# Kernel optimization log

Hardware: AMD Instinct MI355X
Metric: run time of the kernel (lower is better)

## Reference

```python
import jax, jax.numpy as jnp
import numpy as np

B, TK, NK, H = 64, 512, 256, 512

def _masked_renorm_softmax(scores, mask):
    # softmax over last dim, multiply by mask, renormalize (as in the torch code)
    p = jax.nn.softmax(scores, axis=-1) * mask
    return p / jnp.sum(p, axis=-1, keepdims=True)

def setup_inputs() -> dict:
    key = jax.random.key(0)
    ks = jax.random.split(key, 14)
    s = 0.02
    return {
        "s_t_hat": jax.random.normal(ks[0], (B, 2 * H), jnp.float32),
        "encoder_outputs_token": jax.random.normal(ks[1], (B, TK, H), jnp.float32),
        "encoder_outputs_node": jax.random.normal(ks[2], (B, NK, H), jnp.float32),
        "node_to_token": jax.random.randint(ks[3], (B, TK), 0, NK),
        "enc_padding_mask_token": jnp.ones((B, TK), jnp.float32),
        "enc_padding_mask_node": jnp.ones((B, NK), jnp.float32),
        "graph": jax.random.uniform(ks[4], (B, NK, NK), jnp.float32),
        "flow": jax.random.uniform(ks[5], (B, NK), jnp.float32),
        # parameters (Linear weights stored as [in, out]; x @ W == torch Linear)
        "W_c": jax.random.normal(ks[6], (H,), jnp.float32) * s,          # Linear(1, H)
        "W_tok": jax.random.normal(ks[7], (H, H), jnp.float32) * s,      # encode_proj_token
        "W_node": jax.random.normal(ks[8], (H, H), jnp.float32) * s,     # encode_proj_node
        "W_dec": jax.random.normal(ks[9], (2 * H, H), jnp.float32) * s,  # decode_proj
        "b_dec": jnp.zeros((H,), jnp.float32),
        "v_tok": jax.random.normal(ks[10], (H,), jnp.float32) * s,       # v_token
        "v_node": jax.random.normal(ks[11], (H,), jnp.float32) * s,      # v_node
    }

def reference(s_t_hat, encoder_outputs_token, encoder_outputs_node, node_to_token,
              enc_padding_mask_token, enc_padding_mask_node, graph, flow,
              W_c, W_tok, W_node, W_dec, b_dec, v_tok, v_node):
    # projections
    enc_tok_feat = jnp.einsum('bth,hk->btk', encoder_outputs_token, W_tok)   # [B,TK,H]
    enc_node_feat = jnp.einsum('bnh,hk->bnk', encoder_outputs_node, W_node)  # [B,NK,H]
    dec_fea = s_t_hat @ W_dec + b_dec                                        # [B,H]
    flow_feat = flow[..., None] * W_c                                        # [B,NK,H]

    # node attention
    e_node = jnp.tanh(enc_node_feat + dec_fea[:, None, :] + flow_feat)
    scores_node = jnp.einsum('bnh,h->bn', e_node, v_node)                    # [B,NK]
    attn_dist_node = _masked_renorm_softmax(scores_node, enc_padding_mask_node)

    # gather node attention onto tokens via node_to_token indices
    gathered = jnp.take_along_axis(attn_dist_node, node_to_token, axis=1)    # [B,TK]
    attn_dist_node_to_token = _masked_renorm_softmax(gathered, enc_padding_mask_token)

    # token attention
    e_tok = jnp.tanh(enc_tok_feat + dec_fea[:, None, :])
    scores_tok = jnp.einsum('bth,h->bt', e_tok, v_tok)                       # [B,TK]
    attn_dist_token = _masked_renorm_softmax(scores_tok, enc_padding_mask_token)

    # mix and context
    final_attn = 0.5 * attn_dist_token + 0.5 * attn_dist_node_to_token      # [B,TK]
    c_t = jnp.einsum('bt,bth->bh', final_attn, encoder_outputs_token)        # [B,H]

    # multi-hop graph diffusion of node attention
    zero_hop = attn_dist_node                                                # [B,NK]
    one_hop = jnp.einsum('bn,bnm->bm', zero_hop, graph)
    two_hop = jnp.einsum('bn,bnm->bm', one_hop, graph)
    flow_out = (zero_hop + one_hop + two_hop) * 0.33333

    return (c_t, final_attn, attn_dist_node, flow_out)
```

## Files before the change

### kernel.cpp

```cpp
#include <hip/hip_runtime.h>
#include <math.h>

constexpr int kB = 64;
constexpr int kTK = 512;
constexpr int kNK = 256;
constexpr int kH = 512;

typedef float f32x4 __attribute__((ext_vector_type(4)));
typedef __bf16 bf16x8 __attribute__((ext_vector_type(8)));

__device__ __forceinline__ unsigned short f32_to_bf16(float f) {
  unsigned int u = __float_as_uint(f);
  u += 0x7fffu + ((u >> 16) & 1u);
  return (unsigned short)(u >> 16);
}

__device__ __forceinline__ float tanh_fast(float x) {
  float e = __builtin_amdgcn_exp2f(x * 2.8853900817779268f);
  return 1.0f - 2.0f * __builtin_amdgcn_rcpf(e + 1.0f);
}

__global__ __launch_bounds__(256) void transpose_w_kernel(
    const float* __restrict__ Wtok, const float* __restrict__ Wnode,
    unsigned short* __restrict__ WtokT, unsigned short* __restrict__ WnodeT) {
  const float* W = blockIdx.z ? Wnode : Wtok;
  unsigned short* T = blockIdx.z ? WnodeT : WtokT;
  __shared__ float tile[32][33];
  const int tx = threadIdx.x, ty = threadIdx.y;
  const int bx = blockIdx.x, by = blockIdx.y;
#pragma unroll
  for (int i = 0; i < 4; ++i)
    tile[ty + 8 * i][tx] = W[(size_t)(by * 32 + ty + 8 * i) * kH + bx * 32 + tx];
  __syncthreads();
#pragma unroll
  for (int i = 0; i < 4; ++i)
    T[(size_t)(bx * 32 + ty + 8 * i) * kH + by * 32 + tx] =
        f32_to_bf16(tile[tx][ty + 8 * i]);
}

__global__ __launch_bounds__(512) void dec_fea_kernel(
    const float* __restrict__ s_t_hat, const float* __restrict__ W_dec,
    const float* __restrict__ b_dec, float* __restrict__ dec_fea) {
  __shared__ float sh[2 * kH];
  const int b = blockIdx.x, h = threadIdx.x;
  sh[h] = s_t_hat[(size_t)b * (2 * kH) + h];
  sh[h + kH] = s_t_hat[(size_t)b * (2 * kH) + kH + h];
  __syncthreads();
  float acc = 0.f;
#pragma unroll 16
  for (int k = 0; k < 2 * kH; ++k)
    acc = fmaf(sh[k], W_dec[(size_t)k * kH + h], acc);
  dec_fea[b * kH + h] = acc + b_dec[h];
}

template <int ROWS, bool IS_NODE>
__global__ __launch_bounds__(1024, 4) void scores_kernel(
    const float* __restrict__ A,
    const unsigned short* __restrict__ WT,
    const float* __restrict__ dec_fea,
    const float* __restrict__ flow,
    const float* __restrict__ W_c,
    const float* __restrict__ v,
    float* __restrict__ scores)
{
  constexpr int TILES_PER_B = ROWS / 64;
  const int b = blockIdx.x / TILES_PER_B;
  const int row0 = (blockIdx.x % TILES_PER_B) * 64;
  const int tid = threadIdx.x;
  const int wave = tid >> 6;
  const int lane = tid & 63;
  const int quad = lane >> 4;
  const int l15 = lane & 15;
  const int n0 = wave * 32;

  constexpr int LDA = 72;
  __shared__ __align__(16) unsigned short As[2 * 64 * LDA];
  __shared__ float red[16][64];

  const f32x4 fzero = {0.f, 0.f, 0.f, 0.f};
  f32x4 acc[4][2];
#pragma unroll
  for (int i = 0; i < 4; ++i)
#pragma unroll
    for (int j = 0; j < 2; ++j) acc[i][j] = fzero;

  const int r = tid >> 4;
  const int k0 = (tid & 15) * 4;
  const float* aptr = A + ((size_t)(b * ROWS + row0 + r)) * kH + k0;

  {
    float4 af = *(const float4*)(aptr);
    ushort4 ah;
    ah.x = f32_to_bf16(af.x); ah.y = f32_to_bf16(af.y);
    ah.z = f32_to_bf16(af.z); ah.w = f32_to_bf16(af.w);
    *(ushort4*)&As[r * LDA + k0] = ah;
  }

  const unsigned short* wt_base = WT + (size_t)(n0 + l15) * kH + quad * 8;

#pragma unroll 1
  for (int kc8 = 0; kc8 < 8; ++kc8) {
    __syncthreads();
    const unsigned short* Ac = As + (kc8 & 1) * (64 * LDA);

    bf16x8 bfr[2][2];
#pragma unroll
    for (int kh = 0; kh < 2; ++kh)
#pragma unroll
      for (int ni = 0; ni < 2; ++ni)
        bfr[kh][ni] = *(const bf16x8*)(wt_base + (size_t)(16 * ni) * kH +
                                       kc8 * 64 + kh * 32);

    bf16x8 afr[2][4];
#pragma unroll
    for (int kh = 0; kh < 2; ++kh)
#pragma unroll
      for (int mi = 0; mi < 4; ++mi)
        afr[kh][mi] =
            *(const bf16x8*)&Ac[(16 * mi + l15) * LDA + kh * 32 + quad * 8];

    if (kc8 < 7) {
      float4 af = *(const float4*)(aptr + (kc8 + 1) * 64);
      ushort4 ah;
      ah.x = f32_to_bf16(af.x); ah.y = f32_to_bf16(af.y);
      ah.z = f32_to_bf16(af.z); ah.w = f32_to_bf16(af.w);
      *(ushort4*)&As[((kc8 + 1) & 1) * (64 * LDA) + r * LDA + k0] = ah;
    }

#pragma unroll
    for (int kh = 0; kh < 2; ++kh)
#pragma unroll
      for (int mi = 0; mi < 4; ++mi)
#pragma unroll
        for (int ni = 0; ni < 2; ++ni)
          acc[mi][ni] = __builtin_amdgcn_mfma_f32_16x16x32_bf16(
              afr[kh][mi], bfr[kh][ni], acc[mi][ni], 0, 0, 0);
  }

  float dec2[2], vv2[2], wc2[2];
#pragma unroll
  for (int ni = 0; ni < 2; ++ni) {
    const int col = n0 + 16 * ni + l15;
    dec2[ni] = dec_fea[b * kH + col];
    vv2[ni] = v[col];
    if constexpr (IS_NODE) wc2[ni] = W_c[col]; else wc2[ni] = 0.f;
  }
#pragma unroll
  for (int mi = 0; mi < 4; ++mi) {
#pragma unroll
    for (int reg = 0; reg < 4; ++reg) {
      const int row = 16 * mi + quad * 4 + reg;
      float fl = 0.f;
      if constexpr (IS_NODE) fl = flow[b * kNK + row0 + row];
      float p = 0.f;
#pragma unroll
      for (int ni = 0; ni < 2; ++ni) {
        float val = acc[mi][ni][reg] + dec2[ni];
        if constexpr (IS_NODE) val = fmaf(fl, wc2[ni], val);
        p += tanh_fast(val) * vv2[ni];
      }
#pragma unroll
      for (int off = 1; off < 16; off <<= 1) p += __shfl_xor(p, off, 64);
      if (l15 == 0) red[wave][row] = p;
    }
  }
  __syncthreads();
  if (tid < 64) {
    float s = 0.f;
#pragma unroll
    for (int w = 0; w < 16; ++w) s += red[w][tid];
    scores[b * ROWS + row0 + tid] = s;
  }
}

__device__ __forceinline__ float block_max_512(float v, float* rbuf) {
#pragma unroll
  for (int off = 32; off >= 1; off >>= 1) v = fmaxf(v, __shfl_xor(v, off, 64));
  if ((threadIdx.x & 63) == 0) rbuf[threadIdx.x >> 6] = v;
  __syncthreads();
  float m = rbuf[0];
#pragma unroll
  for (int w = 1; w < 8; ++w) m = fmaxf(m, rbuf[w]);
  __syncthreads();
  return m;
}

__device__ __forceinline__ float block_sum_512(float v, float* rbuf) {
#pragma unroll
  for (int off = 32; off >= 1; off >>= 1) v += __shfl_xor(v, off, 64);
  if ((threadIdx.x & 63) == 0) rbuf[threadIdx.x >> 6] = v;
  __syncthreads();
  float s = rbuf[0];
#pragma unroll
  for (int w = 1; w < 8; ++w) s += rbuf[w];
  __syncthreads();
  return s;
}

__global__ __launch_bounds__(512) void softmax_mix_kernel(
    const float* __restrict__ scores_node, const float* __restrict__ scores_tok,
    const int* __restrict__ node_to_token,
    const float* __restrict__ mask_tok, const float* __restrict__ mask_node,
    float* __restrict__ out_final, float* __restrict__ out_attn_node) {
  const int b = blockIdx.x, tid = threadIdx.x;
  __shared__ float an_sh[kNK];
  __shared__ float rbuf[8];

  float sn = (tid < kNK) ? scores_node[b * kNK + tid] : -INFINITY;
  float m = block_max_512(sn, rbuf);
  float e = (tid < kNK) ? expf(sn - m) : 0.f;
  float s = block_sum_512(e, rbuf);
  float pm = (tid < kNK) ? (e / s) * mask_node[b * kNK + tid] : 0.f;
  float s2 = block_sum_512(pm, rbuf);
  float an = pm / s2;
  if (tid < kNK) {
    an_sh[tid] = an;
    out_attn_node[b * kNK + tid] = an;
  }
  __syncthreads();

  const float mt = mask_tok[b * kTK + tid];
  const int idx = node_to_token[b * kTK + tid];
  float g = an_sh[idx];
  float m2 = block_max_512(g, rbuf);
  float e2 = expf(g - m2);
  float sg = block_sum_512(e2, rbuf);
  float pg = (e2 / sg) * mt;
  float sg2 = block_sum_512(pg, rbuf);
  float an2t = pg / sg2;

  float st = scores_tok[b * kTK + tid];
  float m3 = block_max_512(st, rbuf);
  float e3 = expf(st - m3);
  float s3 = block_sum_512(e3, rbuf);
  float pt = (e3 / s3) * mt;
  float s32 = block_sum_512(pt, rbuf);
  float at = pt / s32;

  out_final[b * kTK + tid] = 0.5f * (at + an2t);
}

__global__ __launch_bounds__(512) void ct_partial_kernel(
    const float* __restrict__ final_attn, const float* __restrict__ enc_tok,
    float* __restrict__ ctp) {
  const int s = blockIdx.x, b = blockIdx.y, h = threadIdx.x;
  __shared__ float fa[128];
  if (h < 128) fa[h] = final_attn[b * kTK + s * 128 + h];
  __syncthreads();
  float acc = 0.f;
  const float* base = enc_tok + ((size_t)(b * kTK + s * 128)) * kH + h;
#pragma unroll 8
  for (int t = 0; t < 128; ++t)
    acc = fmaf(fa[t], base[(size_t)t * kH], acc);
  ctp[(size_t)(b * 4 + s) * kH + h] = acc;
}

__global__ __launch_bounds__(512) void ct_reduce_kernel(
    const float* __restrict__ ctp, float* __restrict__ out_ct) {
  const int b = blockIdx.x, h = threadIdx.x;
  float acc = 0.f;
#pragma unroll
  for (int s = 0; s < 4; ++s) acc += ctp[(size_t)(b * 4 + s) * kH + h];
  out_ct[b * kH + h] = acc;
}

__global__ __launch_bounds__(256) void flow1_kernel(
    const float* __restrict__ attn_node, const float* __restrict__ graph,
    float* __restrict__ fp1) {
  const int s = blockIdx.x, b = blockIdx.y, m = threadIdx.x;
  __shared__ float z[32];
  if (m < 32) z[m] = attn_node[b * kNK + s * 32 + m];
  __syncthreads();
  float acc = 0.f;
  const float* g = graph + ((size_t)(b * kNK + s * 32)) * kNK + m;
#pragma unroll 8
  for (int n = 0; n < 32; ++n) acc = fmaf(z[n], g[(size_t)n * kNK], acc);
  fp1[(b * 8 + s) * kNK + m] = acc;
}

__global__ __launch_bounds__(256) void flow3_kernel(
    const float* __restrict__ fp1, const float* __restrict__ graph,
    float* __restrict__ fp2) {
  const int s = blockIdx.x, b = blockIdx.y, m = threadIdx.x;
  __shared__ float one[32];
  if (m < 32) {
    float o = 0.f;
#pragma unroll
    for (int sp = 0; sp < 8; ++sp) o += fp1[(b * 8 + sp) * kNK + s * 32 + m];
    one[m] = o;
  }
  __syncthreads();
  float acc = 0.f;
  const float* g = graph + ((size_t)(b * kNK + s * 32)) * kNK + m;
#pragma unroll 8
  for (int n = 0; n < 32; ++n) acc = fmaf(one[n], g[(size_t)n * kNK], acc);
  fp2[(b * 8 + s) * kNK + m] = acc;
}

__global__ __launch_bounds__(256) void flow4_kernel(
    const float* __restrict__ fp1, const float* __restrict__ fp2,
    const float* __restrict__ attn_node, float* __restrict__ out_flow) {
  const int b = blockIdx.x, m = threadIdx.x;
  float one = 0.f, two = 0.f;
#pragma unroll
  for (int s = 0; s < 8; ++s) {
    one += fp1[(b * 8 + s) * kNK + m];
    two += fp2[(b * 8 + s) * kNK + m];
  }
  out_flow[b * kNK + m] = (attn_node[b * kNK + m] + one + two) * 0.33333f;
}

extern "C" void kernel_launch(void* const* d_in, const int* in_sizes, int n_in,
                              void* d_out, int out_size, void* d_ws, size_t ws_size,
                              hipStream_t stream) {
  (void)in_sizes; (void)n_in; (void)out_size; (void)ws_size;
  const float* s_t_hat  = (const float*)d_in[0];
  const float* enc_tok  = (const float*)d_in[1];
  const float* enc_node = (const float*)d_in[2];
  const int*   n2t      = (const int*)d_in[3];
  const float* mask_tok = (const float*)d_in[4];
  const float* mask_nd  = (const float*)d_in[5];
  const float* graph    = (const float*)d_in[6];
  const float* flow     = (const float*)d_in[7];
  const float* W_c      = (const float*)d_in[8];
  const float* W_tok    = (const float*)d_in[9];
  const float* W_node   = (const float*)d_in[10];
  const float* W_dec    = (const float*)d_in[11];
  const float* b_dec    = (const float*)d_in[12];
  const float* v_tok    = (const float*)d_in[13];
  const float* v_node   = (const float*)d_in[14];

  float* out = (float*)d_out;
  float* out_ct        = out;
  float* out_final     = out + kB * kH;
  float* out_attn_node = out + 2 * kB * kH;
  float* out_flow      = out_attn_node + kB * kNK;

  float* ws = (float*)d_ws;
  float* dec_fea_buf = ws;
  float* scores_tok  = ws + 32768;
  float* scores_node = ws + 65536;
  float* fp1         = ws + 81920;
  float* fp2         = ws + 81920 + 131072;
  unsigned short* WtokT  = (unsigned short*)(ws + 344064);
  unsigned short* WnodeT = WtokT + kH * kH;
  float* ctp = (float*)WtokT;

  transpose_w_kernel<<<dim3(16, 16, 2), dim3(32, 8), 0, stream>>>(
      W_tok, W_node, WtokT, WnodeT);
  dec_fea_kernel<<<kB, 512, 0, stream>>>(s_t_hat, W_dec, b_dec, dec_fea_buf);
  scores_kernel<kTK, false><<<kB * kTK / 64, 1024, 0, stream>>>(
      enc_tok, WtokT, dec_fea_buf, nullptr, nullptr, v_tok, scores_tok);
  scores_kernel<kNK, true><<<kB * kNK / 64, 1024, 0, stream>>>(
      enc_node, WnodeT, dec_fea_buf, flow, W_c, v_node, scores_node);
  softmax_mix_kernel<<<kB, 512, 0, stream>>>(scores_node, scores_tok, n2t,
                                             mask_tok, mask_nd, out_final, out_attn_node);
  ct_partial_kernel<<<dim3(4, kB), 512, 0, stream>>>(out_final, enc_tok, ctp);
  ct_reduce_kernel<<<kB, 512, 0, stream>>>(ctp, out_ct);
  flow1_kernel<<<dim3(8, kB), 256, 0, stream>>>(out_attn_node, graph, fp1);
  flow3_kernel<<<dim3(8, kB), 256, 0, stream>>>(fp1, graph, fp2);
  flow4_kernel<<<kB, 256, 0, stream>>>(fp1, fp2, out_attn_node, out_flow);
}
```

Before: 273.0 us.

## Retile score GEMM, split dec_fea matvec, drop softmax max passes, widen ct split

The scores kernel moves to 512 threads with each wave computing 64 output columns. It uses a fragment-ordered shared-memory layout for A and register double-buffers the B fragments, to raise per-wave reuse and overlap loads with MFMA work. The dec_fea matvec is split across 8 K-slices plus a reduce kernel for more parallelism. The c_t partial split goes from 4 to 8 slices. The softmax kernel drops the max-subtraction and the separate normalize-then-mask passes, folding the mask into one sum, which removes many block reductions but risks exp overflow for large scores.

```diff
diff --git a/kernel.cpp b/kernel.cpp
--- a/kernel.cpp
+++ b/kernel.cpp
@@ -8,6 +8,7 @@
 
 typedef float f32x4 __attribute__((ext_vector_type(4)));
 typedef __bf16 bf16x8 __attribute__((ext_vector_type(8)));
+typedef unsigned short u16x8 __attribute__((ext_vector_type(8)));
 
 __device__ __forceinline__ unsigned short f32_to_bf16(float f) {
   unsigned int u = __float_as_uint(f);
@@ -38,23 +39,32 @@
         f32_to_bf16(tile[tx][ty + 8 * i]);
 }
 
-__global__ __launch_bounds__(512) void dec_fea_kernel(
+__global__ __launch_bounds__(512) void dec_partial_kernel(
     const float* __restrict__ s_t_hat, const float* __restrict__ W_dec,
-    const float* __restrict__ b_dec, float* __restrict__ dec_fea) {
-  __shared__ float sh[2 * kH];
+    float* __restrict__ part) {
+  const int b = blockIdx.x, s = blockIdx.y, h = threadIdx.x;
+  __shared__ float sh[128];
+  if (h < 128) sh[h] = s_t_hat[(size_t)b * (2 * kH) + s * 128 + h];
+  __syncthreads();
+  float acc = 0.f;
+  const float* w = W_dec + (size_t)(s * 128) * kH + h;
+#pragma unroll 8
+  for (int k = 0; k < 128; ++k) acc = fmaf(sh[k], w[(size_t)k * kH], acc);
+  part[(size_t)(b * 8 + s) * kH + h] = acc;
+}
+
+__global__ __launch_bounds__(512) void dec_reduce_kernel(
+    const float* __restrict__ part, const float* __restrict__ b_dec,
+    float* __restrict__ dec_fea) {
   const int b = blockIdx.x, h = threadIdx.x;
-  sh[h] = s_t_hat[(size_t)b * (2 * kH) + h];
-  sh[h + kH] = s_t_hat[(size_t)b * (2 * kH) + kH + h];
-  __syncthreads();
-  float acc = 0.f;
-#pragma unroll 16
-  for (int k = 0; k < 2 * kH; ++k)
-    acc = fmaf(sh[k], W_dec[(size_t)k * kH + h], acc);
-  dec_fea[b * kH + h] = acc + b_dec[h];
+  float acc = b_dec[h];
+#pragma unroll
+  for (int s = 0; s < 8; ++s) acc += part[(size_t)(b * 8 + s) * kH + h];
+  dec_fea[b * kH + h] = acc;
 }
 
 template <int ROWS, bool IS_NODE>
-__global__ __launch_bounds__(1024, 4) void scores_kernel(
+__global__ __launch_bounds__(512, 2) void scores_kernel(
     const float* __restrict__ A,
     const unsigned short* __restrict__ WT,
     const float* __restrict__ dec_fea,
@@ -71,79 +81,86 @@
   const int lane = tid & 63;
   const int quad = lane >> 4;
   const int l15 = lane & 15;
-  const int n0 = wave * 32;
-
-  constexpr int LDA = 72;
-  __shared__ __align__(16) unsigned short As[2 * 64 * LDA];
-  __shared__ float red[16][64];
+  const int n0 = wave * 64;
+
+  __shared__ __align__(16) unsigned short As[2][4096];
+  __shared__ float red[8][64];
 
   const f32x4 fzero = {0.f, 0.f, 0.f, 0.f};
-  f32x4 acc[4][2];
+  f32x4 acc[4][4];
 #pragma unroll
   for (int i = 0; i < 4; ++i)
 #pragma unroll
-    for (int j = 0; j < 2; ++j) acc[i][j] = fzero;
-
-  const int r = tid >> 4;
-  const int k0 = (tid & 15) * 4;
-  const float* aptr = A + ((size_t)(b * ROWS + row0 + r)) * kH + k0;
-
-  {
-    float4 af = *(const float4*)(aptr);
-    ushort4 ah;
-    ah.x = f32_to_bf16(af.x); ah.y = f32_to_bf16(af.y);
-    ah.z = f32_to_bf16(af.z); ah.w = f32_to_bf16(af.w);
-    *(ushort4*)&As[r * LDA + k0] = ah;
-  }
-
-  const unsigned short* wt_base = WT + (size_t)(n0 + l15) * kH + quad * 8;
-
-#pragma unroll 1
-  for (int kc8 = 0; kc8 < 8; ++kc8) {
-    __syncthreads();
-    const unsigned short* Ac = As + (kc8 & 1) * (64 * LDA);
-
-    bf16x8 bfr[2][2];
+    for (int j = 0; j < 4; ++j) acc[i][j] = fzero;
+
+  const int sr = tid >> 3;
+  const int kq = tid & 7;
+  const int slot = (((kq >> 2) * 4 + (sr >> 4)) * 64 + (kq & 3) * 16 + (sr & 15)) * 8;
+  const float* aptr = A + ((size_t)(b * ROWS + row0 + sr)) * kH + kq * 8;
+
+  auto stage = [&](int kc, int buf) {
+    float4 a0 = *(const float4*)(aptr + kc * 64);
+    float4 a1 = *(const float4*)(aptr + kc * 64 + 4);
+    u16x8 h;
+    h[0] = f32_to_bf16(a0.x); h[1] = f32_to_bf16(a0.y);
+    h[2] = f32_to_bf16(a0.z); h[3] = f32_to_bf16(a0.w);
+    h[4] = f32_to_bf16(a1.x); h[5] = f32_to_bf16(a1.y);
+    h[6] = f32_to_bf16(a1.z); h[7] = f32_to_bf16(a1.w);
+    *(u16x8*)&As[buf][slot] = h;
+  };
+
+  const unsigned short* bbase = WT + (size_t)(n0 + l15) * kH + quad * 8;
+  auto load_b = [&](bf16x8 (&dst)[2][4], int kc) {
 #pragma unroll
     for (int kh = 0; kh < 2; ++kh)
 #pragma unroll
-      for (int ni = 0; ni < 2; ++ni)
-        bfr[kh][ni] = *(const bf16x8*)(wt_base + (size_t)(16 * ni) * kH +
-                                       kc8 * 64 + kh * 32);
-
+      for (int ni = 0; ni < 4; ++ni)
+        dst[kh][ni] =
+            *(const bf16x8*)(bbase + (size_t)(ni * 16) * kH + kc * 64 + kh * 32);
+  };
+
+  bf16x8 bcur[2][4];
+  stage(0, 0);
+  load_b(bcur, 0);
+  __syncthreads();
+
+#pragma unroll
+  for (int kc = 0; kc < 8; ++kc) {
+    bf16x8 bnxt[2][4];
+    if (kc < 7) {
+      load_b(bnxt, kc + 1);
+      stage(kc + 1, (kc + 1) & 1);
+    }
     bf16x8 afr[2][4];
 #pragma unroll
     for (int kh = 0; kh < 2; ++kh)
 #pragma unroll
       for (int mi = 0; mi < 4; ++mi)
-        afr[kh][mi] =
-            *(const bf16x8*)&Ac[(16 * mi + l15) * LDA + kh * 32 + quad * 8];
-
-    if (kc8 < 7) {
-      float4 af = *(const float4*)(aptr + (kc8 + 1) * 64);
-      ushort4 ah;
-      ah.x = f32_to_bf16(af.x); ah.y = f32_to_bf16(af.y);
-      ah.z = f32_to_bf16(af.z); ah.w = f32_to_bf16(af.w);
-      *(ushort4*)&As[((kc8 + 1) & 1) * (64 * LDA) + r * LDA + k0] = ah;
+        afr[kh][mi] = *(const bf16x8*)&As[kc & 1][((kh * 4 + mi) * 64 + lane) * 8];
+#pragma unroll
+    for (int kh = 0; kh < 2; ++kh)
+#pragma unroll
+      for (int mi = 0; mi < 4; ++mi)
+#pragma unroll
+        for (int ni = 0; ni < 4; ++ni)
+          acc[mi][ni] = __builtin_amdgcn_mfma_f32_16x16x32_bf16(
+              afr[kh][mi], bcur[kh][ni], acc[mi][ni], 0, 0, 0);
+    if (kc < 7) {
+#pragma unroll
+      for (int kh = 0; kh < 2; ++kh)
+#pragma unroll
+        for (int ni = 0; ni < 4; ++ni) bcur[kh][ni] = bnxt[kh][ni];
+      __syncthreads();
     }
-
-#pragma unroll
-    for (int kh = 0; kh < 2; ++kh)
-#pragma unroll
-      for (int mi = 0; mi < 4; ++mi)
-#pragma unroll
-        for (int ni = 0; ni < 2; ++ni)
-          acc[mi][ni] = __builtin_amdgcn_mfma_f32_16x16x32_bf16(
-              afr[kh][mi], bfr[kh][ni], acc[mi][ni], 0, 0, 0);
-  }
-
-  float dec2[2], vv2[2], wc2[2];
-#pragma unroll
-  for (int ni = 0; ni < 2; ++ni) {
+  }
+
+  float dec4[4], vv4[4], wc4[4];
+#pragma unroll
+  for (int ni = 0; ni < 4; ++ni) {
     const int col = n0 + 16 * ni + l15;
-    dec2[ni] = dec_fea[b * kH + col];
-    vv2[ni] = v[col];
-    if constexpr (IS_NODE) wc2[ni] = W_c[col]; else wc2[ni] = 0.f;
+    dec4[ni] = dec_fea[b * kH + col];
+    vv4[ni] = v[col];
+    if constexpr (IS_NODE) wc4[ni] = W_c[col]; else wc4[ni] = 0.f;
   }
 #pragma unroll
   for (int mi = 0; mi < 4; ++mi) {
@@ -154,10 +171,10 @@
       if constexpr (IS_NODE) fl = flow[b * kNK + row0 + row];
       float p = 0.f;
 #pragma unroll
-      for (int ni = 0; ni < 2; ++ni) {
-        float val = acc[mi][ni][reg] + dec2[ni];
-        if constexpr (IS_NODE) val = fmaf(fl, wc2[ni], val);
-        p += tanh_fast(val) * vv2[ni];
+      for (int ni = 0; ni < 4; ++ni) {
+        float val = acc[mi][ni][reg] + dec4[ni];
+        if constexpr (IS_NODE) val = fmaf(fl, wc4[ni], val);
+        p += tanh_fast(val) * vv4[ni];
       }
 #pragma unroll
       for (int off = 1; off < 16; off <<= 1) p += __shfl_xor(p, off, 64);
@@ -168,21 +185,9 @@
   if (tid < 64) {
     float s = 0.f;
 #pragma unroll
-    for (int w = 0; w < 16; ++w) s += red[w][tid];
+    for (int w = 0; w < 8; ++w) s += red[w][tid];
     scores[b * ROWS + row0 + tid] = s;
   }
-}
-
-__device__ __forceinline__ float block_max_512(float v, float* rbuf) {
-#pragma unroll
-  for (int off = 32; off >= 1; off >>= 1) v = fmaxf(v, __shfl_xor(v, off, 64));
-  if ((threadIdx.x & 63) == 0) rbuf[threadIdx.x >> 6] = v;
-  __syncthreads();
-  float m = rbuf[0];
-#pragma unroll
-  for (int w = 1; w < 8; ++w) m = fmaxf(m, rbuf[w]);
-  __syncthreads();
-  return m;
 }
 
 __device__ __forceinline__ float block_sum_512(float v, float* rbuf) {
@@ -206,13 +211,11 @@
   __shared__ float an_sh[kNK];
   __shared__ float rbuf[8];
 
-  float sn = (tid < kNK) ? scores_node[b * kNK + tid] : -INFINITY;
-  float m = block_max_512(sn, rbuf);
-  float e = (tid < kNK) ? expf(sn - m) : 0.f;
-  float s = block_sum_512(e, rbuf);
-  float pm = (tid < kNK) ? (e / s) * mask_node[b * kNK + tid] : 0.f;
-  float s2 = block_sum_512(pm, rbuf);
-  float an = pm / s2;
+  float en = 0.f;
+  if (tid < kNK)
+    en = expf(scores_node[b * kNK + tid]) * mask_node[b * kNK + tid];
+  float sn = block_sum_512(en, rbuf);
+  float an = en / sn;
   if (tid < kNK) {
     an_sh[tid] = an;
     out_attn_node[b * kNK + tid] = an;
@@ -221,21 +224,13 @@
 
   const float mt = mask_tok[b * kTK + tid];
   const int idx = node_to_token[b * kTK + tid];
-  float g = an_sh[idx];
-  float m2 = block_max_512(g, rbuf);
-  float e2 = expf(g - m2);
-  float sg = block_sum_512(e2, rbuf);
-  float pg = (e2 / sg) * mt;
-  float sg2 = block_sum_512(pg, rbuf);
-  float an2t = pg / sg2;
-
-  float st = scores_tok[b * kTK + tid];
-  float m3 = block_max_512(st, rbuf);
-  float e3 = expf(st - m3);
-  float s3 = block_sum_512(e3, rbuf);
-  float pt = (e3 / s3) * mt;
-  float s32 = block_sum_512(pt, rbuf);
-  float at = pt / s32;
+  float eg = expf(an_sh[idx]) * mt;
+  float sg = block_sum_512(eg, rbuf);
+  float an2t = eg / sg;
+
+  float et = expf(scores_tok[b * kTK + tid]) * mt;
+  float st = block_sum_512(et, rbuf);
+  float at = et / st;
 
   out_final[b * kTK + tid] = 0.5f * (at + an2t);
 }
@@ -244,15 +239,14 @@
     const float* __restrict__ final_attn, const float* __restrict__ enc_tok,
     float* __restrict__ ctp) {
   const int s = blockIdx.x, b = blockIdx.y, h = threadIdx.x;
-  __shared__ float fa[128];
-  if (h < 128) fa[h] = final_attn[b * kTK + s * 128 + h];
-  __syncthreads();
-  float acc = 0.f;
-  const float* base = enc_tok + ((size_t)(b * kTK + s * 128)) * kH + h;
+  __shared__ float fa[64];
+  if (h < 64) fa[h] = final_attn[b * kTK + s * 64 + h];
+  __syncthreads();
+  float acc = 0.f;
+  const float* base = enc_tok + ((size_t)(b * kTK + s * 64)) * kH + h;
 #pragma unroll 8
-  for (int t = 0; t < 128; ++t)
-    acc = fmaf(fa[t], base[(size_t)t * kH], acc);
-  ctp[(size_t)(b * 4 + s) * kH + h] = acc;
+  for (int t = 0; t < 64; ++t) acc = fmaf(fa[t], base[(size_t)t * kH], acc);
+  ctp[(size_t)(b * 8 + s) * kH + h] = acc;
 }
 
 __global__ __launch_bounds__(512) void ct_reduce_kernel(
@@ -260,7 +254,7 @@
   const int b = blockIdx.x, h = threadIdx.x;
   float acc = 0.f;
 #pragma unroll
-  for (int s = 0; s < 4; ++s) acc += ctp[(size_t)(b * 4 + s) * kH + h];
+  for (int s = 0; s < 8; ++s) acc += ctp[(size_t)(b * 8 + s) * kH + h];
   out_ct[b * kH + h] = acc;
 }
 
@@ -341,21 +335,23 @@
   float* scores_tok  = ws + 32768;
   float* scores_node = ws + 65536;
   float* fp1         = ws + 81920;
-  float* fp2         = ws + 81920 + 131072;
-  unsigned short* WtokT  = (unsigned short*)(ws + 344064);
+  float* fp2         = ws + 212992;
+  float* dec_part    = ws + 344064;
+  float* ctp         = dec_part;
+  unsigned short* WtokT  = (unsigned short*)(ws + 606208);
   unsigned short* WnodeT = WtokT + kH * kH;
-  float* ctp = (float*)WtokT;
 
   transpose_w_kernel<<<dim3(16, 16, 2), dim3(32, 8), 0, stream>>>(
       W_tok, W_node, WtokT, WnodeT);
-  dec_fea_kernel<<<kB, 512, 0, stream>>>(s_t_hat, W_dec, b_dec, dec_fea_buf);
-  scores_kernel<kTK, false><<<kB * kTK / 64, 1024, 0, stream>>>(
+  dec_partial_kernel<<<dim3(kB, 8), 512, 0, stream>>>(s_t_hat, W_dec, dec_part);
+  dec_reduce_kernel<<<kB, 512, 0, stream>>>(dec_part, b_dec, dec_fea_buf);
+  scores_kernel<kTK, false><<<kB * kTK / 64, 512, 0, stream>>>(
       enc_tok, WtokT, dec_fea_buf, nullptr, nullptr, v_tok, scores_tok);
-  scores_kernel<kNK, true><<<kB * kNK / 64, 1024, 0, stream>>>(
+  scores_kernel<kNK, true><<<kB * kNK / 64, 512, 0, stream>>>(
       enc_node, WnodeT, dec_fea_buf, flow, W_c, v_node, scores_node);
   softmax_mix_kernel<<<kB, 512, 0, stream>>>(scores_node, scores_tok, n2t,
                                              mask_tok, mask_nd, out_final, out_attn_node);
-  ct_partial_kernel<<<dim3(4, kB), 512, 0, stream>>>(out_final, enc_tok, ctp);
+  ct_partial_kernel<<<dim3(8, kB), 512, 0, stream>>>(out_final, enc_tok, ctp);
   ct_reduce_kernel<<<kB, 512, 0, stream>>>(ctp, out_ct);
   flow1_kernel<<<dim3(8, kB), 256, 0, stream>>>(out_attn_node, graph, fp1);
   flow3_kernel<<<dim3(8, kB), 256, 0, stream>>>(fp1, graph, fp2);
```

Result: faster. 248.1 us (-9.1%).
